# Performance work log

Measured on AMD Instinct MI355X. Metric: run time of the kernel, lower is better.

Reference implementation:

```python
import jax, jax.numpy as jnp
import numpy as np

B, S, D_MODEL, H = 2, 2048, 2048, 16
HEAD_DIM = D_MODEL // H  # 128


def setup_inputs() -> dict:
    key = jax.random.key(0)
    k1, k2, k3 = jax.random.split(key, 3)
    x = jax.random.normal(k1, (B, S, D_MODEL), dtype=jnp.float32)
    Wqkv = jax.random.normal(k2, (D_MODEL, 3 * D_MODEL), dtype=jnp.float32) * (D_MODEL ** -0.5)
    Wout = jax.random.normal(k3, (D_MODEL, D_MODEL), dtype=jnp.float32) * (D_MODEL ** -0.5)
    return {"x": x, "Wqkv": Wqkv, "Wout": Wout}


def reference(x, Wqkv, Wout):
    b, s, _ = x.shape
    # QKV projection: (B, S, 3*H*D) -> (B, S, 3, H, D)
    qkv = (x @ Wqkv).reshape(b, s, 3, H, HEAD_DIM)
    q, k, v = qkv[:, :, 0], qkv[:, :, 1], qkv[:, :, 2]
    scale = HEAD_DIM ** -0.5
    # scores: (B, H, Sq, Sk)
    scores = jnp.einsum("bqhd,bkhd->bhqk", q, k) * scale
    causal = jnp.arange(s)[:, None] >= jnp.arange(s)[None, :]
    scores = jnp.where(causal[None, None, :, :], scores, -1e9)
    attn = jax.nn.softmax(scores, axis=-1)
    out = jnp.einsum("bhqk,bkhd->bqhd", attn, v)  # (B, S, H, D)
    out = out.reshape(b, s, D_MODEL)
    return out @ Wout
```

## Files before the change

kernel.cpp:

```cpp
#include <hip/hip_runtime.h>
#include <hip/hip_bf16.h>


#define SEQ 2048
#define DM 2048
#define NQKV 6144
#define DH 128

typedef __attribute__((ext_vector_type(8))) short bf16x8;
typedef __attribute__((ext_vector_type(4))) float f32x4;

__device__ __forceinline__ f32x4 mfma16(bf16x8 a, bf16x8 b, f32x4 c) {
  return __builtin_amdgcn_mfma_f32_16x16x32_bf16(a, b, c, 0, 0, 0);
}

__device__ __forceinline__ void gload_lds16(const void* g, void* l) {
  __builtin_amdgcn_global_load_lds(
      (const __attribute__((address_space(1))) unsigned int*)g,
      (__attribute__((address_space(3))) unsigned int*)l, 16, 0, 0);
}

__global__ __launch_bounds__(256) void cast_f32_bf16(
    const float* __restrict__ in, __hip_bfloat16* __restrict__ out, int n4) {
  int i = blockIdx.x * 256 + threadIdx.x;
  if (i >= n4) return;
  float4 f = reinterpret_cast<const float4*>(in)[i];
  union { __hip_bfloat16 h[4]; unsigned long long u; } o;
  o.h[0] = __float2bfloat16(f.x); o.h[1] = __float2bfloat16(f.y);
  o.h[2] = __float2bfloat16(f.z); o.h[3] = __float2bfloat16(f.w);
  reinterpret_cast<unsigned long long*>(out)[i] = o.u;
}

__global__ __launch_bounds__(256) void transpose_cast(
    const float* __restrict__ in, __hip_bfloat16* __restrict__ out, int R, int C) {
  __shared__ float t[32][33];
  int c0 = blockIdx.x * 32, r0 = blockIdx.y * 32;
  int tx = threadIdx.x, ty = threadIdx.y;
#pragma unroll
  for (int i = 0; i < 4; ++i)
    t[ty + i * 8][tx] = in[(size_t)(r0 + ty + i * 8) * C + c0 + tx];
  __syncthreads();
#pragma unroll
  for (int i = 0; i < 4; ++i)
    out[(size_t)(c0 + ty + i * 8) * R + r0 + tx] = __float2bfloat16(t[tx][ty + i * 8]);
}

__global__ __launch_bounds__(256) void transpose_v(
    const __hip_bfloat16* __restrict__ qkv, __hip_bfloat16* __restrict__ vT) {
  __shared__ __hip_bfloat16 t[32][33];
  int bh = blockIdx.z;
  int b = bh >> 4, h = bh & 15;
  int s0 = blockIdx.x * 32, d0 = blockIdx.y * 32;
  int tx = threadIdx.x, ty = threadIdx.y;
#pragma unroll
  for (int i = 0; i < 4; ++i)
    t[ty + i * 8][tx] =
        qkv[(size_t)(b * SEQ + s0 + ty + i * 8) * NQKV + 2 * DM + h * DH + d0 + tx];
  __syncthreads();
#pragma unroll
  for (int i = 0; i < 4; ++i)
    vT[(size_t)(bh * DH + d0 + ty + i * 8) * SEQ + s0 + tx] = t[tx][ty + i * 8];
}

template <int EPI>
__global__ __launch_bounds__(256) void gemm_bt(
    const __hip_bfloat16* __restrict__ A, const __hip_bfloat16* __restrict__ Bt,
    void* __restrict__ Cout, int M, int N, int K) {
  __shared__ alignas(16) __hip_bfloat16 As[128 * 64];
  __shared__ alignas(16) __hip_bfloat16 Bs[128 * 64];
  const int tid = threadIdx.x;
  const int lane = tid & 63;
  const int w = tid >> 6, wr = w >> 1, wc = w & 1;
  const int lr = lane & 15, lg = lane >> 4;
  const int m0 = blockIdx.y * 128, n0 = blockIdx.x * 128;
  f32x4 acc[4][4] = {};
  for (int k0 = 0; k0 < K; k0 += 64) {
#pragma unroll
    for (int it = 0; it < 4; ++it) {
      int e = (it * 256 + tid) * 8;
      int row = e >> 6, col = e & 63;
      gload_lds16(A + (size_t)(m0 + row) * K + k0 + col, (char*)As + (size_t)e * 2);
      gload_lds16(Bt + (size_t)(n0 + row) * K + k0 + col, (char*)Bs + (size_t)e * 2);
    }
    __syncthreads();
#pragma unroll
    for (int ks = 0; ks < 2; ++ks) {
      bf16x8 af[4], bfr[4];
#pragma unroll
      for (int m = 0; m < 4; ++m)
        af[m] = *(const bf16x8*)((const char*)As +
                                 (wr * 64 + m * 16 + lr) * 128 + ks * 64 + lg * 16);
#pragma unroll
      for (int n = 0; n < 4; ++n)
        bfr[n] = *(const bf16x8*)((const char*)Bs +
                                  (wc * 64 + n * 16 + lr) * 128 + ks * 64 + lg * 16);
#pragma unroll
      for (int m = 0; m < 4; ++m)
#pragma unroll
        for (int n = 0; n < 4; ++n)
          acc[m][n] = mfma16(af[m], bfr[n], acc[m][n]);
    }
    __syncthreads();
  }
  const int crow = m0 + wr * 64, ccol = n0 + wc * 64;
#pragma unroll
  for (int m = 0; m < 4; ++m)
#pragma unroll
    for (int n = 0; n < 4; ++n)
#pragma unroll
      for (int j = 0; j < 4; ++j) {
        int r = crow + m * 16 + lg * 4 + j;
        int c = ccol + n * 16 + lr;
        if (EPI == 0)
          ((__hip_bfloat16*)Cout)[(size_t)r * N + c] = __float2bfloat16(acc[m][n][j]);
        else
          ((float*)Cout)[(size_t)r * N + c] = acc[m][n][j];
      }
}

__device__ __forceinline__ void attn_tile(
    const bf16x8 (&qf)[4], f32x4 (&of)[8], float (&mrun)[4], float (&lrun)[4],
    const char* Ks, const char* Vs, char* pw,
    int lr, int lg, int kv0, int myq, bool lastmask, float scale) {
  f32x4 sacc[8];
#pragma unroll
  for (int n = 0; n < 8; ++n) sacc[n] = f32x4{0.f, 0.f, 0.f, 0.f};
#pragma unroll
  for (int n = 0; n < 8; ++n) {
    const int krow = n * 16 + lr;
    const char* kbase = Ks + krow * 256;
#pragma unroll
    for (int ks = 0; ks < 4; ++ks) {
      int c = ks * 64 + lg * 16;
      bf16x8 kb = *(const bf16x8*)(kbase + (c ^ ((krow & 7) << 4)));
      sacc[n] = mfma16(qf[ks], kb, sacc[n]);
    }
  }
#pragma unroll
  for (int n = 0; n < 8; ++n)
#pragma unroll
    for (int j = 0; j < 4; ++j) {
      float v = sacc[n][j] * scale;
      if (lastmask && (kv0 + n * 16 + lr > myq + j)) v = -1e30f;
      sacc[n][j] = v;
    }
  float pm[4];
#pragma unroll
  for (int j = 0; j < 4; ++j) {
    float a = fmaxf(fmaxf(sacc[0][j], sacc[1][j]), fmaxf(sacc[2][j], sacc[3][j]));
    float bx = fmaxf(fmaxf(sacc[4][j], sacc[5][j]), fmaxf(sacc[6][j], sacc[7][j]));
    pm[j] = fmaxf(a, bx);
  }
#pragma unroll
  for (int d = 1; d < 16; d <<= 1)
#pragma unroll
    for (int j = 0; j < 4; ++j) pm[j] = fmaxf(pm[j], __shfl_xor(pm[j], d));
  bool big = false;
#pragma unroll
  for (int j = 0; j < 4; ++j) big = big || (pm[j] > mrun[j] + 8.0f);
  if (__any(big)) {
#pragma unroll
    for (int j = 0; j < 4; ++j) {
      float mn = fmaxf(mrun[j], pm[j]);
      float corr = __expf(mrun[j] - mn);
      mrun[j] = mn;
      lrun[j] *= corr;
#pragma unroll
      for (int nn = 0; nn < 8; ++nn) of[nn][j] *= corr;
    }
  }
  float rs[4] = {0.f, 0.f, 0.f, 0.f};
#pragma unroll
  for (int n = 0; n < 8; ++n)
#pragma unroll
    for (int j = 0; j < 4; ++j) {
      float pv = __expf(sacc[n][j] - mrun[j]);
      sacc[n][j] = pv;
      rs[j] += pv;
    }
#pragma unroll
  for (int d = 1; d < 16; d <<= 1)
#pragma unroll
    for (int j = 0; j < 4; ++j) rs[j] += __shfl_xor(rs[j], d);
#pragma unroll
  for (int j = 0; j < 4; ++j) lrun[j] += rs[j];
#pragma unroll
  for (int j = 0; j < 4; ++j) {
    int prow = lg * 4 + j;
    char* pb = pw + prow * 256;
#pragma unroll
    for (int n = 0; n < 8; ++n) {
      int c = (n * 16 + lr) * 2;
      *(__hip_bfloat16*)(pb + (c ^ ((prow & 7) << 4))) = __float2bfloat16(sacc[n][j]);
    }
  }
#pragma unroll
  for (int kvs = 0; kvs < 4; ++kvs) {
    int c = kvs * 64 + lg * 16;
    bf16x8 pa = *(const bf16x8*)(pw + lr * 256 + (c ^ ((lr & 7) << 4)));
#pragma unroll
    for (int nn = 0; nn < 8; ++nn) {
      int vrow = nn * 16 + lr;
      bf16x8 vb = *(const bf16x8*)(Vs + vrow * 256 + (c ^ ((vrow & 7) << 4)));
      of[nn] = mfma16(pa, vb, of[nn]);
    }
  }
}

__global__ __launch_bounds__(256, 2) void attn_causal(
    const __hip_bfloat16* __restrict__ qkv, const __hip_bfloat16* __restrict__ vT,
    __hip_bfloat16* __restrict__ O) {
  __shared__ alignas(16) __hip_bfloat16 Ks[128 * 128];
  __shared__ alignas(16) __hip_bfloat16 Vs[128 * 128];
  __shared__ alignas(16) __hip_bfloat16 Ps[4][16 * 128];
  const int tid = threadIdx.x, lane = tid & 63, w = tid >> 6;
  const int lr = lane & 15, lg = lane >> 4;
  const int p = blockIdx.x, bh = blockIdx.y;
  const int b = bh >> 4, h = bh & 15;
  const int qtA = p, qtB = 31 - p;
  const int q0A = qtA * 64, q0B = qtB * 64;
  const int ntA = (qtA + 2) >> 1, ntB = (qtB + 2) >> 1;
  const float scale = 0.08838834764831845f;
  bf16x8 qfA[4], qfB[4];
  {
    const __hip_bfloat16* qpA =
        qkv + (size_t)(b * SEQ + q0A + w * 16 + lr) * NQKV + h * DH;
    const __hip_bfloat16* qpB =
        qkv + (size_t)(b * SEQ + q0B + w * 16 + lr) * NQKV + h * DH;
#pragma unroll
    for (int ks = 0; ks < 4; ++ks) {
      qfA[ks] = *(const bf16x8*)(qpA + ks * 32 + lg * 8);
      qfB[ks] = *(const bf16x8*)(qpB + ks * 32 + lg * 8);
    }
  }
  f32x4 ofA[8] = {}, ofB[8] = {};
  float mA[4], lA[4], mB[4], lB[4];
#pragma unroll
  for (int j = 0; j < 4; ++j) { mA[j] = mB[j] = -1e30f; lA[j] = lB[j] = 0.f; }
  const int myqA = q0A + w * 16 + lg * 4;
  const int myqB = q0B + w * 16 + lg * 4;
  char* pw = (char*)&Ps[w][0];

  for (int t = 0; t < ntB; ++t) {
    const int kv0 = t * 128;
#pragma unroll
    for (int it = 0; it < 8; ++it) {
      int g = it * 256 + tid;
      int r = g >> 4, sl = g & 15;
      int ssl = sl ^ (r & 7);
      gload_lds16(qkv + (size_t)(b * SEQ + kv0 + r) * NQKV + DM + h * DH + ssl * 8,
                  (char*)Ks + (size_t)g * 16);
    }
#pragma unroll
    for (int it = 0; it < 8; ++it) {
      int g = it * 256 + tid;
      int r = g >> 4, sl = g & 15;
      int ssl = sl ^ (r & 7);
      gload_lds16(vT + (size_t)(bh * DH + r) * SEQ + kv0 + ssl * 8,
                  (char*)Vs + (size_t)g * 16);
    }
    __syncthreads();
    if (t < ntA)
      attn_tile(qfA, ofA, mA, lA, (const char*)Ks, (const char*)Vs, pw,
                lr, lg, kv0, myqA, t == ntA - 1, scale);
    attn_tile(qfB, ofB, mB, lB, (const char*)Ks, (const char*)Vs, pw,
              lr, lg, kv0, myqB, t == ntB - 1, scale);
    __syncthreads();
  }
#pragma unroll
  for (int j = 0; j < 4; ++j) {
    float invA = 1.0f / lA[j], invB = 1.0f / lB[j];
    __hip_bfloat16* opA =
        O + (size_t)(b * SEQ + q0A + w * 16 + lg * 4 + j) * DM + h * DH;
    __hip_bfloat16* opB =
        O + (size_t)(b * SEQ + q0B + w * 16 + lg * 4 + j) * DM + h * DH;
#pragma unroll
    for (int nn = 0; nn < 8; ++nn) {
      opA[nn * 16 + lr] = __float2bfloat16(ofA[nn][j] * invA);
      opB[nn * 16 + lr] = __float2bfloat16(ofB[nn][j] * invB);
    }
  }
}

extern "C" void kernel_launch(void* const* d_in, const int* in_sizes, int n_in,
                              void* d_out, int out_size, void* d_ws, size_t ws_size,
                              hipStream_t stream) {
  const float* x = (const float*)d_in[0];
  const float* Wqkv = (const float*)d_in[1];
  const float* Wout = (const float*)d_in[2];
  float* out = (float*)d_out;
  char* ws = (char*)d_ws;
  __hip_bfloat16* xb    = (__hip_bfloat16*)(ws + 0);
  __hip_bfloat16* wqkvT = (__hip_bfloat16*)(ws + (size_t)16777216);
  __hip_bfloat16* woutT = (__hip_bfloat16*)(ws + (size_t)41943040);
  __hip_bfloat16* qkvb  = (__hip_bfloat16*)(ws + (size_t)50331648);
  __hip_bfloat16* vT    = (__hip_bfloat16*)(ws + (size_t)100663296);
  __hip_bfloat16* ob    = (__hip_bfloat16*)(ws + (size_t)117440512);

  cast_f32_bf16<<<dim3(8192), dim3(256), 0, stream>>>(x, xb, 8388608 / 4);
  transpose_cast<<<dim3(192, 64), dim3(32, 8), 0, stream>>>(Wqkv, wqkvT, 2048, 6144);
  transpose_cast<<<dim3(64, 64), dim3(32, 8), 0, stream>>>(Wout, woutT, 2048, 2048);
  gemm_bt<0><<<dim3(48, 32), dim3(256), 0, stream>>>(xb, wqkvT, qkvb, 4096, 6144, 2048);
  transpose_v<<<dim3(64, 4, 32), dim3(32, 8), 0, stream>>>(qkvb, vT);
  attn_causal<<<dim3(16, 32), dim3(256), 0, stream>>>(qkvb, vT, ob);
  gemm_bt<1><<<dim3(16, 32), dim3(256), 0, stream>>>(ob, woutT, out, 4096, 2048, 2048);
}
```

Before: 435.2 us.

## Replace GEMM with 256x256-tile double-buffered pipelined kernel using swizzled LDS

Replaces the 128x128 single-buffered GEMM with a 256x256 tile kernel using 8 waves, double-buffered LDS, and four-phase interleaving that issues the next K-tile's global loads while running MFMAs on the current one. LDS uses an XOR swizzle to avoid bank conflicts. Blocks are remapped across an 8-way chiplet-style swizzle for L2 locality. s_setprio is raised around the MFMA runs. The aim is to hide memory latency and raise arithmetic intensity in both projections. The cost is hand-tuned vmcnt waits that must exactly match the load order, and fewer blocks (384 and 128) for a 256-CU device.

```diff
diff --git a/kernel.cpp b/kernel.cpp
--- a/kernel.cpp
+++ b/kernel.cpp
@@ -63,58 +63,100 @@
 }
 
 template <int EPI>
-__global__ __launch_bounds__(256) void gemm_bt(
+__global__ __launch_bounds__(512, 2) void gemm256(
     const __hip_bfloat16* __restrict__ A, const __hip_bfloat16* __restrict__ Bt,
     void* __restrict__ Cout, int M, int N, int K) {
-  __shared__ alignas(16) __hip_bfloat16 As[128 * 64];
-  __shared__ alignas(16) __hip_bfloat16 Bs[128 * 64];
+  __shared__ alignas(16) char lds[131072];
   const int tid = threadIdx.x;
-  const int lane = tid & 63;
-  const int w = tid >> 6, wr = w >> 1, wc = w & 1;
+  const int lane = tid & 63, w = tid >> 6;
+  const int wm = w >> 2, wn = w & 3;
   const int lr = lane & 15, lg = lane >> 4;
-  const int m0 = blockIdx.y * 128, n0 = blockIdx.x * 128;
-  f32x4 acc[4][4] = {};
-  for (int k0 = 0; k0 < K; k0 += 64) {
-#pragma unroll
-    for (int it = 0; it < 4; ++it) {
-      int e = (it * 256 + tid) * 8;
-      int row = e >> 6, col = e & 63;
-      gload_lds16(A + (size_t)(m0 + row) * K + k0 + col, (char*)As + (size_t)e * 2);
-      gload_lds16(Bt + (size_t)(n0 + row) * K + k0 + col, (char*)Bs + (size_t)e * 2);
-    }
-    __syncthreads();
-#pragma unroll
-    for (int ks = 0; ks < 2; ++ks) {
-      bf16x8 af[4], bfr[4];
-#pragma unroll
-      for (int m = 0; m < 4; ++m)
-        af[m] = *(const bf16x8*)((const char*)As +
-                                 (wr * 64 + m * 16 + lr) * 128 + ks * 64 + lg * 16);
-#pragma unroll
-      for (int n = 0; n < 4; ++n)
-        bfr[n] = *(const bf16x8*)((const char*)Bs +
-                                  (wc * 64 + n * 16 + lr) * 128 + ks * 64 + lg * 16);
-#pragma unroll
-      for (int m = 0; m < 4; ++m)
-#pragma unroll
-        for (int n = 0; n < 4; ++n)
-          acc[m][n] = mfma16(af[m], bfr[n], acc[m][n]);
-    }
-    __syncthreads();
-  }
-  const int crow = m0 + wr * 64, ccol = n0 + wc * 64;
-#pragma unroll
-  for (int m = 0; m < 4; ++m)
-#pragma unroll
-    for (int n = 0; n < 4; ++n)
+  const int nbn = N >> 8;
+  const int cpx = gridDim.x >> 3;
+  const int swz = (blockIdx.x & 7) * cpx + (blockIdx.x >> 3);
+  const size_t bm0 = (size_t)(swz / nbn) << 8;
+  const size_t bn0 = (size_t)(swz % nbn) << 8;
+  const int nt = K >> 6;
+
+  const int r0 = tid >> 3;
+  const int scol = ((tid & 7) ^ (r0 & 7)) * 8;
+  const int laneA = wm * 8192 + lr * 128;
+  const int laneB = wn * 4096 + lr * 128;
+  const int s0 = (lg ^ (lr & 7)) * 16;
+  const int s1 = ((4 + lg) ^ (lr & 7)) * 16;
+
+  f32x4 acc[8][4] = {};
+
+  auto STAGE = [&](int which, int kt) {
+    char* dst = lds + (which >> 1) * 65536 + (kt & 1) * 32768 +
+                (which & 1) * 16384 + tid * 16;
+    const __hip_bfloat16* src = (which >= 2) ? Bt : A;
+    size_t rbase = ((which >= 2) ? bn0 : bm0) + (size_t)((which & 1) * 128);
+    int kc = kt * 64 + scol;
+#pragma unroll
+    for (int i = 0; i < 2; ++i)
+      gload_lds16(src + (rbase + r0 + i * 64) * K + kc, dst + i * 8192);
+  };
+
+#define PHASE(MH, NH, STW, VMTAIL)                                             \
+  do {                                                                         \
+    const int par = (t & 1) * 32768;                                           \
+    bf16x8 af[4][2], bq[2][2];                                                 \
+    _Pragma("unroll") for (int mf = 0; mf < 4; ++mf) {                         \
+      const char* ab = lds + par + (MH)*16384 + laneA + mf * 2048;             \
+      af[mf][0] = *(const bf16x8*)(ab + s0);                                   \
+      af[mf][1] = *(const bf16x8*)(ab + s1);                                   \
+    }                                                                          \
+    _Pragma("unroll") for (int nf = 0; nf < 2; ++nf) {                         \
+      const char* bb = lds + 65536 + par + (NH)*16384 + laneB + nf * 2048;     \
+      bq[nf][0] = *(const bf16x8*)(bb + s0);                                   \
+      bq[nf][1] = *(const bf16x8*)(bb + s1);                                   \
+    }                                                                          \
+    if (t + 1 < nt) {                                                          \
+      STAGE(STW, t + 1);                                                       \
+      asm volatile("s_waitcnt vmcnt(4)" ::: "memory");                         \
+    } else if ((VMTAIL) == 2) {                                                \
+      asm volatile("s_waitcnt vmcnt(2)" ::: "memory");                         \
+    } else if ((VMTAIL) == 0) {                                                \
+      asm volatile("s_waitcnt vmcnt(0)" ::: "memory");                         \
+    }                                                                          \
+    __builtin_amdgcn_s_barrier();                                              \
+    __builtin_amdgcn_sched_barrier(0);                                         \
+    __builtin_amdgcn_s_setprio(1);                                             \
+    _Pragma("unroll") for (int ks = 0; ks < 2; ++ks)                           \
+        _Pragma("unroll") for (int mf = 0; mf < 4; ++mf)                       \
+        _Pragma("unroll") for (int nf = 0; nf < 2; ++nf)                       \
+            acc[(MH)*4 + mf][(NH)*2 + nf] = mfma16(                            \
+            af[mf][ks], bq[nf][ks], acc[(MH)*4 + mf][(NH)*2 + nf]);            \
+    __builtin_amdgcn_s_setprio(0);                                             \
+    __builtin_amdgcn_sched_barrier(0);                                         \
+    __builtin_amdgcn_s_barrier();                                              \
+  } while (0)
+
+  STAGE(0, 0); STAGE(2, 0); STAGE(3, 0); STAGE(1, 0);
+  asm volatile("s_waitcnt vmcnt(4)" ::: "memory");
+  __builtin_amdgcn_s_barrier();
+
+  for (int t = 0; t < nt; ++t) {
+    PHASE(0, 0, 0, 2);
+    PHASE(0, 1, 2, 0);
+    PHASE(1, 0, 3, -1);
+    PHASE(1, 1, 1, -1);
+  }
+#undef PHASE
+
+#pragma unroll
+  for (int mi = 0; mi < 8; ++mi)
+#pragma unroll
+    for (int ni = 0; ni < 4; ++ni)
 #pragma unroll
       for (int j = 0; j < 4; ++j) {
-        int r = crow + m * 16 + lg * 4 + j;
-        int c = ccol + n * 16 + lr;
+        size_t r = bm0 + (mi >> 2) * 128 + wm * 64 + (mi & 3) * 16 + lg * 4 + j;
+        size_t c = bn0 + (ni >> 1) * 128 + wn * 32 + (ni & 1) * 16 + lr;
         if (EPI == 0)
-          ((__hip_bfloat16*)Cout)[(size_t)r * N + c] = __float2bfloat16(acc[m][n][j]);
+          ((__hip_bfloat16*)Cout)[r * N + c] = __float2bfloat16(acc[mi][ni][j]);
         else
-          ((float*)Cout)[(size_t)r * N + c] = acc[m][n][j];
+          ((float*)Cout)[r * N + c] = acc[mi][ni][j];
       }
 }
 
@@ -300,8 +342,8 @@
   cast_f32_bf16<<<dim3(8192), dim3(256), 0, stream>>>(x, xb, 8388608 / 4);
   transpose_cast<<<dim3(192, 64), dim3(32, 8), 0, stream>>>(Wqkv, wqkvT, 2048, 6144);
   transpose_cast<<<dim3(64, 64), dim3(32, 8), 0, stream>>>(Wout, woutT, 2048, 2048);
-  gemm_bt<0><<<dim3(48, 32), dim3(256), 0, stream>>>(xb, wqkvT, qkvb, 4096, 6144, 2048);
+  gemm256<0><<<dim3(384), dim3(512), 0, stream>>>(xb, wqkvT, qkvb, 4096, 6144, 2048);
   transpose_v<<<dim3(64, 4, 32), dim3(32, 8), 0, stream>>>(qkvb, vT);
   attn_causal<<<dim3(16, 32), dim3(256), 0, stream>>>(qkvb, vT, ob);
-  gemm_bt<1><<<dim3(16, 32), dim3(256), 0, stream>>>(ob, woutT, out, 4096, 2048, 2048);
-}
+  gemm256<1><<<dim3(128), dim3(512), 0, stream>>>(ob, woutT, out, 4096, 2048, 2048);
+}
```

Measured after the change: 443.7 us. About the same (+1.9%).
